# Kernel tuning notes

Measured on AMD Instinct MI355X. Metric: run time of the kernel, lower is better.

## Reference

```python
import jax, jax.numpy as jnp
import numpy as np

N = 100000
E = 1600000
IN_C = 128
OUT_C = 32
HEADS = 4
NEG_SLOPE = 0.2


def setup_inputs() -> dict:
    key = jax.random.key(0)
    k1, k2, k3, k4, k5 = jax.random.split(key, 5)
    x = jax.random.normal(k1, (N, IN_C), dtype=jnp.float32)
    edge_index = jax.random.randint(k2, (2, E), 0, N, dtype=jnp.int64)
    # Xavier-ish scaled params
    W = jax.random.normal(k3, (OUT_C * HEADS, IN_C), dtype=jnp.float32) * (1.414 * np.sqrt(2.0 / (IN_C + OUT_C * HEADS)))
    att_l = jax.random.normal(k4, (1, HEADS, OUT_C), dtype=jnp.float32) * 0.1
    att_r = jax.random.normal(k5, (1, HEADS, OUT_C), dtype=jnp.float32) * 0.1
    bias = jnp.zeros((OUT_C * HEADS,), dtype=jnp.float32)
    return {"x": x, "edge_index": edge_index, "W": W, "att_l": att_l, "att_r": att_r, "bias": bias}


def reference(x, edge_index, W, att_l, att_r, bias):
    row, col = edge_index[0], edge_index[1]
    # per-node projection: [N, H, C]
    x_proj = (x @ W.T).reshape(N, HEADS, OUT_C)
    x_i = x_proj[row]          # [E, H, C] gather by source
    x_j = x_proj[col]          # [E, H, C] gather by target
    alpha = (x_i * att_l).sum(-1) + (x_j * att_r).sum(-1)   # [E, H]
    alpha = jnp.where(alpha >= 0, alpha, NEG_SLOPE * alpha)  # leaky_relu
    # edge softmax grouped by row (faithful: plain exp, eps=1e-16)
    alpha_exp = jnp.exp(alpha)
    denom = jax.ops.segment_sum(alpha_exp, row, num_segments=N)  # [N, H]
    alpha = alpha_exp / (denom[row] + 1e-16)
    # weighted scatter-add over all heads at once: [N, H, C]
    out = jax.ops.segment_sum(x_j * alpha[:, :, None], row, num_segments=N)
    out = out.reshape(N, HEADS * OUT_C) + bias
    return out
```

## Files before the change

kernel.cpp:

```cpp
#include <hip/hip_runtime.h>
#include <hip/hip_fp16.h>


constexpr float NEG_SLOPE = 0.2f;
constexpr int TILE_ROWS = 64;
constexpr int SLAB = 2048;
constexpr int EPB = 8192;
constexpr int NB_PAD = 2048;
constexpr int FBMAX = 256;

typedef __attribute__((ext_vector_type(8))) short short8;
typedef __attribute__((ext_vector_type(4))) float f32x4;

__device__ inline short f2bf(float f) {
    unsigned u = __float_as_uint(f);
    return (short)((u + 0x7fffu + ((u >> 16) & 1u)) >> 16);
}

__global__ __launch_bounds__(512) void k_fg(const float* __restrict__ x,
                                            const float* __restrict__ W,
                                            const float* __restrict__ attl,
                                            const float* __restrict__ attr,
                                            const int* __restrict__ ei,
                                            __half* __restrict__ xph,
                                            float* __restrict__ l,
                                            float* __restrict__ r,
                                            unsigned int* __restrict__ slab,
                                            int* __restrict__ starts,
                                            int N, int E, int NB, int FB, int S) {
    __shared__ __align__(16) char smem[49152];
    __shared__ float s_att[256];
    __shared__ int s_wsum[8];
    int t = threadIdx.x;
    int lane = t & 63, wv = t >> 6;
    int b = blockIdx.x;
    bool isfill = (b % S == 0) && (b / S < FB);

    if (isfill) {
        int* s_hist = (int*)smem;
        int* s_cur  = (int*)(smem + 8192);
        unsigned int* s_stage = (unsigned int*)(smem + 16384);

        int fb = b / S;
        int e0 = fb * EPB;
        int ecnt = min(EPB, E - e0);
        bool full = (ecnt == EPB) && ((E & 3) == 0);

        for (int i = t; i < NB_PAD; i += 512) s_hist[i] = 0;
        __syncthreads();

        const int* rows = ei;
        const int* cols = ei + E;

        if (full) {
            const int4* r4 = (const int4*)rows + (e0 >> 2);
#pragma unroll
            for (int k = 0; k < 4; ++k) {
                int4 ra = r4[k * 512 + t];
                atomicAdd(&s_hist[ra.x >> 6], 1);
                atomicAdd(&s_hist[ra.y >> 6], 1);
                atomicAdd(&s_hist[ra.z >> 6], 1);
                atomicAdd(&s_hist[ra.w >> 6], 1);
            }
        } else {
            for (int j = t; j < ecnt; j += 512)
                atomicAdd(&s_hist[rows[e0 + j] >> 6], 1);
        }
        __syncthreads();

        int b0 = t * 4;
        int c0 = s_hist[b0], c1 = s_hist[b0 + 1], c2 = s_hist[b0 + 2], c3 = s_hist[b0 + 3];
        int p = c0 + c1 + c2 + c3;
        int v = p;
#pragma unroll
        for (int off = 1; off < 64; off <<= 1) {
            int u = __shfl_up(v, off);
            if (lane >= off) v += u;
        }
        if (lane == 63) s_wsum[wv] = v;
        __syncthreads();
        if (t == 0) {
            int run = 0;
#pragma unroll
            for (int w = 0; w < 8; ++w) { int tmp = s_wsum[w]; s_wsum[w] = run; run += tmp; }
        }
        __syncthreads();
        int base = s_wsum[wv] + (v - p);
        int e1 = base + c0, e2 = e1 + c1, e3 = e2 + c2;
        s_hist[b0] = base; s_hist[b0 + 1] = e1; s_hist[b0 + 2] = e2; s_hist[b0 + 3] = e3;
        s_cur[b0] = base;  s_cur[b0 + 1] = e1;  s_cur[b0 + 2] = e2;  s_cur[b0 + 3] = e3;
        size_t sb = (size_t)fb * (NB + 1);
        if (b0 + 0 <= NB) starts[sb + b0 + 0] = base;
        if (b0 + 1 <= NB) starts[sb + b0 + 1] = e1;
        if (b0 + 2 <= NB) starts[sb + b0 + 2] = e2;
        if (b0 + 3 <= NB) starts[sb + b0 + 3] = e3;
        __syncthreads();

        if (full) {
            const int4* r4 = (const int4*)rows + (e0 >> 2);
            const int4* c4 = (const int4*)cols + (e0 >> 2);
#pragma unroll
            for (int k = 0; k < 4; ++k) {
                int4 ra = r4[k * 512 + t];
                int4 ca = c4[k * 512 + t];
                int pos;
                pos = atomicAdd(&s_cur[ra.x >> 6], 1);
                s_stage[pos] = ((unsigned int)ca.x << 6) | (unsigned int)(ra.x & 63);
                pos = atomicAdd(&s_cur[ra.y >> 6], 1);
                s_stage[pos] = ((unsigned int)ca.y << 6) | (unsigned int)(ra.y & 63);
                pos = atomicAdd(&s_cur[ra.z >> 6], 1);
                s_stage[pos] = ((unsigned int)ca.z << 6) | (unsigned int)(ra.z & 63);
                pos = atomicAdd(&s_cur[ra.w >> 6], 1);
                s_stage[pos] = ((unsigned int)ca.w << 6) | (unsigned int)(ra.w & 63);
            }
        } else {
            for (int j = t; j < ecnt; j += 512) {
                int rr = rows[e0 + j], cc = cols[e0 + j];
                int pos = atomicAdd(&s_cur[rr >> 6], 1);
                s_stage[pos] = ((unsigned int)cc << 6) | (unsigned int)(rr & 63);
            }
        }
        __syncthreads();

        uint4* dst = (uint4*)(slab + (size_t)fb * EPB);
        const uint4* src = (const uint4*)s_stage;
        int n4 = (ecnt + 3) >> 2;
        for (int i = t; i < n4; i += 512) dst[i] = src[i];
        return;
    }

    short* s_wa = (short*)smem;
    if (t < 128)       s_att[t] = attl[t];
    else if (t < 256)  s_att[t] = attr[t - 128];
    for (int i = t; i < 128 * 128; i += 512) {
        int row = i >> 7, col = i & 127;
        s_wa[row * 136 + col] = f2bf(W[i]);
    }
    for (int i = t; i < 1024; i += 512) {
        int row = 136 + (i >> 7), col = i & 127;
        s_wa[row * 136 + col] = 0;
    }
    __syncthreads();
#pragma unroll
    for (int s = 0; s < 2; ++s) {
        int e = t + s * 512;
        int which = e >> 9;
        int h = (e >> 7) & 3;
        int k = e & 127;
        float acc = 0.f;
#pragma unroll 8
        for (int c = 0; c < 32; ++c)
            acc += s_att[which * 128 + h * 32 + c] * W[(h * 32 + c) * 128 + k];
        s_wa[(128 + which * 4 + h) * 136 + k] = f2bf(acc);
    }
    __syncthreads();

    int li = lane & 15, quad = lane >> 4;
    int gb = b - min((b + S - 1) / S, FB);
    int base = gb * 128 + wv * 16;

    f32x4 acc[9];
#pragma unroll
    for (int nt = 0; nt < 9; ++nt) acc[nt] = (f32x4){0.f, 0.f, 0.f, 0.f};

    int anode = base + li;
    bool avalid = anode < N;
    const float4* x4 = (const float4*)x;
    const short8* wb8 = (const short8*)s_wa;

#pragma unroll
    for (int kc = 0; kc < 4; ++kc) {
        float4 p0 = make_float4(0.f, 0.f, 0.f, 0.f), p1 = p0;
        if (avalid) {
            p0 = x4[(size_t)anode * 32 + kc * 8 + quad * 2];
            p1 = x4[(size_t)anode * 32 + kc * 8 + quad * 2 + 1];
        }
        short8 a;
        a[0] = f2bf(p0.x); a[1] = f2bf(p0.y); a[2] = f2bf(p0.z); a[3] = f2bf(p0.w);
        a[4] = f2bf(p1.x); a[5] = f2bf(p1.y); a[6] = f2bf(p1.z); a[7] = f2bf(p1.w);
#pragma unroll
        for (int nt = 0; nt < 9; ++nt) {
            short8 bfrag = wb8[(nt * 16 + li) * 17 + kc * 4 + quad];
            acc[nt] = __builtin_amdgcn_mfma_f32_16x16x32_bf16(a, bfrag, acc[nt], 0, 0, 0);
        }
    }

#pragma unroll
    for (int j = 0; j < 4; ++j) {
        int node = base + quad * 4 + j;
        if (node >= N) continue;
        if (li < 4)      l[node * 4 + li] = acc[8][j];
        else if (li < 8) r[node * 4 + li - 4] = acc[8][j];
    }

    __syncthreads();
    __half* s_out = (__half*)s_wa;
#pragma unroll
    for (int j = 0; j < 4; ++j) {
        int nl = wv * 16 + quad * 4 + j;
#pragma unroll
        for (int nt = 0; nt < 8; ++nt)
            s_out[nl * 136 + nt * 16 + li] = __float2half(acc[nt][j]);
    }
    __syncthreads();
    {
        int nl = t >> 2, seg = t & 3;
        int node = gb * 128 + nl;
        if (node < N) {
            const short8* sr = (const short8*)s_wa;
            short8* xp8 = (short8*)xph;
#pragma unroll
            for (int q = 0; q < 4; ++q)
                xp8[(size_t)node * 16 + seg * 4 + q] = sr[nl * 17 + seg * 4 + q];
        }
    }
}

__global__ __launch_bounds__(512) void k_tile(const int* __restrict__ starts,
                                              const unsigned int* __restrict__ slab,
                                              const float* __restrict__ l,
                                              const float* __restrict__ r,
                                              const __half* __restrict__ xph,
                                              const float* __restrict__ bias,
                                              float* __restrict__ out,
                                              int N, int NB, int FB) {
    __shared__ unsigned int s_packed[SLAB];
    __shared__ int s_col[SLAB];
    __shared__ __half s_w[SLAB * 4];
    __shared__ float s_dsum[TILE_ROWS * 4];
    __shared__ float s_l[TILE_ROWS * 4];
    __shared__ int s_start[TILE_ROWS + 1];
    __shared__ int s_cursor[TILE_ROWS];
    __shared__ int s_cnt[TILE_ROWS];
    __shared__ int s_fbase[FBMAX];
    __shared__ int s_foff[FBMAX + 1];
    __shared__ int s_w4[4];

    int b = blockIdx.x;
    int base = b * TILE_ROWS;
    int t = threadIdx.x;
    int lane = t & 63, wv = t >> 6;
    int rows = min(TILE_ROWS, N - base);

    if (t < TILE_ROWS) s_cnt[t] = 0;
    if (t < rows * 4) s_l[t] = l[base * 4 + t];

    int myc = 0;
    if (t < FB) {
        const int* sp = starts + (size_t)t * (NB + 1) + b;
        int a0 = sp[0], a1 = sp[1];
        s_fbase[t] = a0;
        myc = a1 - a0;
    }
    int v = 0;
    if (t < 256) {
        v = myc;
#pragma unroll
        for (int off = 1; off < 64; off <<= 1) {
            int u = __shfl_up(v, off);
            if (lane >= off) v += u;
        }
        if (lane == 63) s_w4[wv] = v;
    }
    __syncthreads();
    if (t == 0) {
        int run = 0;
#pragma unroll
        for (int w = 0; w < 4; ++w) { int tmp = s_w4[w]; s_w4[w] = run; run += tmp; }
        s_foff[0] = 0;
    }
    __syncthreads();
    if (t < 256) s_foff[t + 1] = v + s_w4[wv];
    __syncthreads();
    int tot = s_foff[FB];
    if (tot > SLAB) tot = SLAB;

    for (int i = t; i < tot; i += 512) {
        int lo = 0, hi = FB;
        while (hi - lo > 1) {
            int mid = (lo + hi) >> 1;
            if (s_foff[mid] <= i) lo = mid; else hi = mid;
        }
        unsigned int p = slab[(size_t)lo * EPB + s_fbase[lo] + (i - s_foff[lo])];
        s_packed[i] = p;
        atomicAdd(&s_cnt[p & 63], 1);
    }
    __syncthreads();

    if (t < 64) {
        int c = s_cnt[t];
        int vv = c;
#pragma unroll
        for (int off = 1; off < 64; off <<= 1) {
            int u = __shfl_up(vv, off);
            if (t >= off) vv += u;
        }
        s_start[t + 1] = vv;
        if (t == 0) s_start[0] = 0;
        s_cursor[t] = vv - c;
    }
    __syncthreads();

    {
        int row_[4], col_[4];
        bool val_[4];
#pragma unroll
        for (int s = 0; s < 4; ++s) {
            int i = t + s * 512;
            bool valid = i < tot;
            unsigned int p = valid ? s_packed[i] : 0u;
            row_[s] = (int)(p & 63);
            col_[s] = valid ? (int)(p >> 6) : 0;
            val_[s] = valid;
        }
        float4 rv0 = ((const float4*)r)[col_[0]];
        float4 rv1 = ((const float4*)r)[col_[1]];
        float4 rv2 = ((const float4*)r)[col_[2]];
        float4 rv3 = ((const float4*)r)[col_[3]];
#pragma unroll
        for (int s = 0; s < 4; ++s) {
            if (!val_[s]) continue;
            float4 rv = s == 0 ? rv0 : s == 1 ? rv1 : s == 2 ? rv2 : rv3;
            int row = row_[s];
            int pos = atomicAdd(&s_cursor[row], 1);
            s_col[pos] = col_[s];
            float4 lv = ((const float4*)s_l)[row];
            float w0 = lv.x + rv.x, w1 = lv.y + rv.y;
            float w2 = lv.z + rv.z, w3 = lv.w + rv.w;
            w0 = w0 >= 0.f ? w0 : NEG_SLOPE * w0;
            w1 = w1 >= 0.f ? w1 : NEG_SLOPE * w1;
            w2 = w2 >= 0.f ? w2 : NEG_SLOPE * w2;
            w3 = w3 >= 0.f ? w3 : NEG_SLOPE * w3;
            w0 = __expf(w0); w1 = __expf(w1); w2 = __expf(w2); w3 = __expf(w3);
            ((__half2*)s_w)[pos * 2]     = __floats2half2_rn(w0, w1);
            ((__half2*)s_w)[pos * 2 + 1] = __floats2half2_rn(w2, w3);
        }
    }
    __syncthreads();

    if (t < 256) {
        int row = t >> 2, h = t & 3;
        if (row < rows) {
            int s0 = s_start[row], s1 = s_start[row + 1];
            float d = 0.f;
            for (int i = s0; i < s1; ++i)
                d += __half2float(s_w[i * 4 + h]);
            s_dsum[t] = d;
        }
    }
    __syncthreads();

    int quarter = lane >> 4;
    int li = lane & 15;
    int h = li >> 2;
    const float4* xp4g = (const float4*)xph;

    float4 b0 = ((const float4*)bias)[2 * li];
    float4 b1 = ((const float4*)bias)[2 * li + 1];

    for (int rl = wv; rl < rows; rl += 8) {
        int s0 = s_start[rl], s1 = s_start[rl + 1];
        float a0 = 0.f, a1 = 0.f, a2 = 0.f, a3 = 0.f;
        float a4 = 0.f, a5 = 0.f, a6 = 0.f, a7 = 0.f;
        for (int i0 = s0 + quarter; i0 < s1; i0 += 16) {
            int i1 = i0 + 4, i2 = i0 + 8, i3 = i0 + 12;
            bool v1 = i1 < s1, v2 = i2 < s1, v3 = i3 < s1;
            int c0 = s_col[i0];
            int c1 = v1 ? s_col[i1] : c0;
            int c2 = v2 ? s_col[i2] : c0;
            int c3 = v3 ? s_col[i3] : c0;
            float w0 = __half2float(s_w[i0 * 4 + h]);
            float w1 = v1 ? __half2float(s_w[i1 * 4 + h]) : 0.f;
            float w2 = v2 ? __half2float(s_w[i2 * 4 + h]) : 0.f;
            float w3 = v3 ? __half2float(s_w[i3 * 4 + h]) : 0.f;
            float4 r0 = xp4g[(size_t)c0 * 16 + li];
            float4 r1 = xp4g[(size_t)c1 * 16 + li];
            float4 r2 = xp4g[(size_t)c2 * 16 + li];
            float4 r3 = xp4g[(size_t)c3 * 16 + li];
#define ACC8(raw, w)                                         \
            {                                                \
                __half2* hp = (__half2*)&(raw);              \
                float2 f0 = __half22float2(hp[0]);           \
                float2 f1 = __half22float2(hp[1]);           \
                float2 f2 = __half22float2(hp[2]);           \
                float2 f3 = __half22float2(hp[3]);           \
                a0 += (w) * f0.x; a1 += (w) * f0.y;          \
                a2 += (w) * f1.x; a3 += (w) * f1.y;          \
                a4 += (w) * f2.x; a5 += (w) * f2.y;          \
                a6 += (w) * f3.x; a7 += (w) * f3.y;          \
            }
            ACC8(r0, w0);
            ACC8(r1, w1);
            ACC8(r2, w2);
            ACC8(r3, w3);
#undef ACC8
        }
        a0 += __shfl_xor(a0, 16); a0 += __shfl_xor(a0, 32);
        a1 += __shfl_xor(a1, 16); a1 += __shfl_xor(a1, 32);
        a2 += __shfl_xor(a2, 16); a2 += __shfl_xor(a2, 32);
        a3 += __shfl_xor(a3, 16); a3 += __shfl_xor(a3, 32);
        a4 += __shfl_xor(a4, 16); a4 += __shfl_xor(a4, 32);
        a5 += __shfl_xor(a5, 16); a5 += __shfl_xor(a5, 32);
        a6 += __shfl_xor(a6, 16); a6 += __shfl_xor(a6, 32);
        a7 += __shfl_xor(a7, 16); a7 += __shfl_xor(a7, 32);
        if (quarter == 0) {
            float inv = 1.f / (s_dsum[rl * 4 + h] + 1e-16f);
            float4 o0, o1;
            o0.x = a0 * inv + b0.x; o0.y = a1 * inv + b0.y;
            o0.z = a2 * inv + b0.z; o0.w = a3 * inv + b0.w;
            o1.x = a4 * inv + b1.x; o1.y = a5 * inv + b1.y;
            o1.z = a6 * inv + b1.z; o1.w = a7 * inv + b1.w;
            ((float4*)out)[(size_t)(base + rl) * 32 + 2 * li] = o0;
            ((float4*)out)[(size_t)(base + rl) * 32 + 2 * li + 1] = o1;
        }
    }
}

extern "C" void kernel_launch(void* const* d_in, const int* in_sizes, int n_in,
                              void* d_out, int out_size, void* d_ws, size_t ws_size,
                              hipStream_t stream) {
    const float* x    = (const float*)d_in[0];
    const int*   ei   = (const int*)d_in[1];
    const float* W    = (const float*)d_in[2];
    const float* attl = (const float*)d_in[3];
    const float* attr = (const float*)d_in[4];
    const float* bias = (const float*)d_in[5];
    int N = in_sizes[0] / 128;
    int E = in_sizes[1] / 2;
    int NB = (N + TILE_ROWS - 1) / TILE_ROWS;
    int FB = (E + EPB - 1) / EPB;

    char* ws = (char*)d_ws;
    __half* xph = (__half*)ws;   ws += (size_t)N * 128 * 2;
    float* l    = (float*)ws;    ws += (size_t)N * 4 * 4;
    float* r    = (float*)ws;    ws += (size_t)N * 4 * 4;
    int* starts = (int*)ws;      ws += (size_t)FB * (NB + 1) * 4;
    unsigned int* slab = (unsigned int*)ws; ws += (size_t)FB * EPB * 4;

    float* out = (float*)d_out;
    int GB = (N + 127) / 128;
    int TOT = FB + GB;
    int S = TOT / FB; if (S < 1) S = 1;

    k_fg<<<TOT, 512, 0, stream>>>(x, W, attl, attr, ei, xph, l, r, slab, starts,
                                  N, E, NB, FB, S);
    k_tile<<<NB, 512, 0, stream>>>(starts, slab, l, r, xph, bias, out, N, NB, FB);
}
```

Measured before the change: 206.4 us.

## Shrink k_tile to 256 threads and keep packed edges in registers

k_tile now launches with 256 threads per block (launch bounds 256, 4) instead of 512. Each thread gathers 8 packed edges into registers rather than staging them through the shared s_packed array, which is removed. The r loads are batched 8-wide, and the accumulate macro now uses explicit fmaf on per-element half conversions. The aim is to cut LDS usage and block size so more blocks fit per CU, at the cost of more registers per thread and fewer waves per row tile.

```diff
diff --git a/kernel.cpp b/kernel.cpp
--- a/kernel.cpp
+++ b/kernel.cpp
@@ -216,15 +216,14 @@
     }
 }
 
-__global__ __launch_bounds__(512) void k_tile(const int* __restrict__ starts,
-                                              const unsigned int* __restrict__ slab,
-                                              const float* __restrict__ l,
-                                              const float* __restrict__ r,
-                                              const __half* __restrict__ xph,
-                                              const float* __restrict__ bias,
-                                              float* __restrict__ out,
-                                              int N, int NB, int FB) {
-    __shared__ unsigned int s_packed[SLAB];
+__global__ __launch_bounds__(256, 4) void k_tile(const int* __restrict__ starts,
+                                                 const unsigned int* __restrict__ slab,
+                                                 const float* __restrict__ l,
+                                                 const float* __restrict__ r,
+                                                 const __half* __restrict__ xph,
+                                                 const float* __restrict__ bias,
+                                                 float* __restrict__ out,
+                                                 int N, int NB, int FB) {
     __shared__ int s_col[SLAB];
     __shared__ __half s_w[SLAB * 4];
     __shared__ float s_dsum[TILE_ROWS * 4];
@@ -252,16 +251,13 @@
         s_fbase[t] = a0;
         myc = a1 - a0;
     }
-    int v = 0;
-    if (t < 256) {
-        v = myc;
-#pragma unroll
-        for (int off = 1; off < 64; off <<= 1) {
-            int u = __shfl_up(v, off);
-            if (lane >= off) v += u;
-        }
-        if (lane == 63) s_w4[wv] = v;
-    }
+    int v = myc;
+#pragma unroll
+    for (int off = 1; off < 64; off <<= 1) {
+        int u = __shfl_up(v, off);
+        if (lane >= off) v += u;
+    }
+    if (lane == 63) s_w4[wv] = v;
     __syncthreads();
     if (t == 0) {
         int run = 0;
@@ -270,21 +266,28 @@
         s_foff[0] = 0;
     }
     __syncthreads();
-    if (t < 256) s_foff[t + 1] = v + s_w4[wv];
+    s_foff[t + 1] = v + s_w4[wv];
     __syncthreads();
     int tot = s_foff[FB];
     if (tot > SLAB) tot = SLAB;
 
-    for (int i = t; i < tot; i += 512) {
-        int lo = 0, hi = FB;
-        while (hi - lo > 1) {
-            int mid = (lo + hi) >> 1;
-            if (s_foff[mid] <= i) lo = mid; else hi = mid;
-        }
-        unsigned int p = slab[(size_t)lo * EPB + s_fbase[lo] + (i - s_foff[lo])];
-        s_packed[i] = p;
-        atomicAdd(&s_cnt[p & 63], 1);
-    }
+    unsigned int pk[8];
+#pragma unroll
+    for (int s = 0; s < 8; ++s) {
+        int i = t + s * 256;
+        pk[s] = 0xFFFFFFFFu;
+        if (i < tot) {
+            int lo = 0, hi = FB;
+            while (hi - lo > 1) {
+                int mid = (lo + hi) >> 1;
+                if (s_foff[mid] <= i) lo = mid; else hi = mid;
+            }
+            pk[s] = slab[(size_t)lo * EPB + s_fbase[lo] + (i - s_foff[lo])];
+        }
+    }
+#pragma unroll
+    for (int s = 0; s < 8; ++s)
+        if (pk[s] != 0xFFFFFFFFu) atomicAdd(&s_cnt[pk[s] & 63], 1);
     __syncthreads();
 
     if (t < 64) {
@@ -302,31 +305,24 @@
     __syncthreads();
 
     {
-        int row_[4], col_[4];
-        bool val_[4];
-#pragma unroll
-        for (int s = 0; s < 4; ++s) {
-            int i = t + s * 512;
-            bool valid = i < tot;
-            unsigned int p = valid ? s_packed[i] : 0u;
-            row_[s] = (int)(p & 63);
-            col_[s] = valid ? (int)(p >> 6) : 0;
-            val_[s] = valid;
-        }
-        float4 rv0 = ((const float4*)r)[col_[0]];
-        float4 rv1 = ((const float4*)r)[col_[1]];
-        float4 rv2 = ((const float4*)r)[col_[2]];
-        float4 rv3 = ((const float4*)r)[col_[3]];
-#pragma unroll
-        for (int s = 0; s < 4; ++s) {
-            if (!val_[s]) continue;
-            float4 rv = s == 0 ? rv0 : s == 1 ? rv1 : s == 2 ? rv2 : rv3;
+        int row_[8], col_[8];
+#pragma unroll
+        for (int s = 0; s < 8; ++s) {
+            row_[s] = (int)(pk[s] & 63);
+            col_[s] = (pk[s] != 0xFFFFFFFFu) ? (int)(pk[s] >> 6) : 0;
+        }
+        float4 rv[8];
+#pragma unroll
+        for (int s = 0; s < 8; ++s) rv[s] = ((const float4*)r)[col_[s]];
+#pragma unroll
+        for (int s = 0; s < 8; ++s) {
+            if (pk[s] == 0xFFFFFFFFu) continue;
             int row = row_[s];
             int pos = atomicAdd(&s_cursor[row], 1);
             s_col[pos] = col_[s];
             float4 lv = ((const float4*)s_l)[row];
-            float w0 = lv.x + rv.x, w1 = lv.y + rv.y;
-            float w2 = lv.z + rv.z, w3 = lv.w + rv.w;
+            float w0 = lv.x + rv[s].x, w1 = lv.y + rv[s].y;
+            float w2 = lv.z + rv[s].z, w3 = lv.w + rv[s].w;
             w0 = w0 >= 0.f ? w0 : NEG_SLOPE * w0;
             w1 = w1 >= 0.f ? w1 : NEG_SLOPE * w1;
             w2 = w2 >= 0.f ? w2 : NEG_SLOPE * w2;
@@ -338,7 +334,7 @@
     }
     __syncthreads();
 
-    if (t < 256) {
+    {
         int row = t >> 2, h = t & 3;
         if (row < rows) {
             int s0 = s_start[row], s1 = s_start[row + 1];
@@ -358,7 +354,7 @@
     float4 b0 = ((const float4*)bias)[2 * li];
     float4 b1 = ((const float4*)bias)[2 * li + 1];
 
-    for (int rl = wv; rl < rows; rl += 8) {
+    for (int rl = wv; rl < rows; rl += 4) {
         int s0 = s_start[rl], s1 = s_start[rl + 1];
         float a0 = 0.f, a1 = 0.f, a2 = 0.f, a3 = 0.f;
         float a4 = 0.f, a5 = 0.f, a6 = 0.f, a7 = 0.f;
@@ -377,17 +373,17 @@
             float4 r1 = xp4g[(size_t)c1 * 16 + li];
             float4 r2 = xp4g[(size_t)c2 * 16 + li];
             float4 r3 = xp4g[(size_t)c3 * 16 + li];
-#define ACC8(raw, w)                                         \
-            {                                                \
-                __half2* hp = (__half2*)&(raw);              \
-                float2 f0 = __half22float2(hp[0]);           \
-                float2 f1 = __half22float2(hp[1]);           \
-                float2 f2 = __half22float2(hp[2]);           \
-                float2 f3 = __half22float2(hp[3]);           \
-                a0 += (w) * f0.x; a1 += (w) * f0.y;          \
-                a2 += (w) * f1.x; a3 += (w) * f1.y;          \
-                a4 += (w) * f2.x; a5 += (w) * f2.y;          \
-                a6 += (w) * f3.x; a7 += (w) * f3.y;          \
+#define ACC8(raw, w)                                             \
+            {                                                    \
+                const __half* hp = (const __half*)&(raw);        \
+                a0 = fmaf((w), __half2float(hp[0]), a0);         \
+                a1 = fmaf((w), __half2float(hp[1]), a1);         \
+                a2 = fmaf((w), __half2float(hp[2]), a2);         \
+                a3 = fmaf((w), __half2float(hp[3]), a3);         \
+                a4 = fmaf((w), __half2float(hp[4]), a4);         \
+                a5 = fmaf((w), __half2float(hp[5]), a5);         \
+                a6 = fmaf((w), __half2float(hp[6]), a6);         \
+                a7 = fmaf((w), __half2float(hp[7]), a7);         \
             }
             ACC8(r0, w0);
             ACC8(r1, w1);
@@ -444,5 +440,5 @@
 
     k_fg<<<TOT, 512, 0, stream>>>(x, W, attl, attr, ei, xph, l, r, slab, starts,
                                   N, E, NB, FB, S);
-    k_tile<<<NB, 512, 0, stream>>>(starts, slab, l, r, xph, bias, out, N, NB, FB);
+    k_tile<<<NB, 256, 0, stream>>>(starts, slab, l, r, xph, bias, out, N, NB, FB);
 }
```

Measured after the change: 214.8 us. 1.04x slower.
